# Kernel tuning notes

Hardware: AMD Instinct MI355X
Metric: run time of the kernel (lower is better)

The kernel has to match this reference:

```python
import jax, jax.numpy as jnp
import numpy as np

N, K, M, C, OUT, S = 80000, 8, 1000, 128, 64, 2
EPS = 1e-5


def _bn(x, g, b, m, v):
    # eval-mode BatchNorm1d applied over the last (channel) axis
    return (x - m) * (g / jnp.sqrt(v + EPS)) + b


def setup_inputs() -> dict:
    key = jax.random.key(0)
    ks = jax.random.split(key, 40)
    it = iter(range(40))
    rn = lambda sh, s=1.0: jax.random.normal(ks[next(it)], sh, dtype=jnp.float32) * s
    ru = lambda sh: jax.random.uniform(ks[next(it)], sh, dtype=jnp.float32, minval=0.5, maxval=1.5)
    w = 0.05
    inp = {}
    inp["sp_fea"] = rn((M, C))
    inp["sp_xyz"] = rn((M, 3))
    inp["o_p_fea"] = rn((N, C))
    inp["p_xyz"] = rn((N, 3))
    # linear_q / linear_k / linear_v  (in_planes -> mid_planes)
    inp["Wq"] = rn((C, C), w); inp["bq"] = jnp.zeros((C,), jnp.float32)
    inp["Wk"] = rn((C, C), w); inp["bk"] = jnp.zeros((C,), jnp.float32)
    inp["Wv"] = rn((C, C), w); inp["bv"] = jnp.zeros((C,), jnp.float32)
    # linear_p: Linear(3,3) -> BN(3) -> ReLU -> Linear(3, mid)
    inp["Wp1"] = rn((3, 3), 0.5); inp["bp1"] = jnp.zeros((3,), jnp.float32)
    inp["gp"] = 1.0 + rn((3,), 0.1); inp["betap"] = rn((3,), 0.1)
    inp["mp"] = rn((3,), 0.1); inp["vp"] = ru((3,))
    inp["Wp2"] = rn((3, C), 0.3); inp["bp2"] = jnp.zeros((C,), jnp.float32)
    # linear_w: BN(mid) -> ReLU -> Linear(mid,out) -> BN(out) -> ReLU -> Linear(out,out)
    inp["g1"] = 1.0 + rn((C,), 0.1); inp["beta1"] = rn((C,), 0.1)
    inp["m1"] = rn((C,), 0.1); inp["v1"] = ru((C,))
    inp["W1"] = rn((C, OUT), w); inp["b1"] = jnp.zeros((OUT,), jnp.float32)
    inp["g2"] = 1.0 + rn((OUT,), 0.1); inp["beta2"] = rn((OUT,), 0.1)
    inp["m2"] = rn((OUT,), 0.1); inp["v2"] = ru((OUT,))
    inp["W2"] = rn((OUT, OUT), w); inp["b2"] = jnp.zeros((OUT,), jnp.float32)
    # index / offset inputs (ints)
    inp["c2p_idx_abs"] = jax.random.randint(ks[next(it)], (N, K), 0, M)
    inp["c2p_idx"] = jax.random.randint(ks[next(it)], (N, K), 0, M)
    inp["cluster_idx"] = jax.random.randint(ks[next(it)], (N,), 0, M)
    inp["offset"] = jnp.array([N], dtype=jnp.int32)
    inp["sp_offset"] = jnp.array([M], dtype=jnp.int32)
    return inp


def reference(sp_fea, sp_xyz, o_p_fea, p_xyz,
              Wq, bq, Wk, bk, Wv, bv,
              Wp1, bp1, gp, betap, mp, vp, Wp2, bp2,
              g1, beta1, m1, v1, W1, b1,
              g2, beta2, m2, v2, W2, b2,
              c2p_idx_abs, c2p_idx, cluster_idx, offset, sp_offset):
    q = o_p_fea @ Wq + bq                               # [N, C]
    k_sp = (sp_fea @ Wk + bk)[c2p_idx_abs]              # gather -> [N, K, C]
    v_sp = (sp_fea @ Wv + bv)[c2p_idx_abs]              # [N, K, C]
    p_e = sp_xyz[c2p_idx_abs]                           # [N, K, 3]
    # positional encoding MLP
    p_e = jax.nn.relu(_bn(p_e @ Wp1 + bp1, gp, betap, mp, vp)) @ Wp2 + bp2  # [N, K, C]
    # vector attention scores
    w = k_sp - q[:, None, :] + p_e                      # [N, K, C]
    w = jax.nn.relu(_bn(w, g1, beta1, m1, v1)) @ W1 + b1
    w = jax.nn.relu(_bn(w, g2, beta2, m2, v2)) @ W2 + b2  # [N, K, OUT]
    w = jax.nn.softmax(w, axis=1)                        # softmax over the K neighbors
    # shared-plane weighted sum
    bi = ((v_sp + p_e).reshape(N, K, S, C // S) * w[:, :, None, :]).reshape(N, K, C)
    bi = bi.sum(axis=2)                                  # [N, K]
    return jax.nn.softmax(bi, axis=1)                    # association matrix [N, K]
```

## Files before the change

### kernel.cpp

```cpp
#include <hip/hip_runtime.h>
#include <stdint.h>

#define EPS 1e-5f

#define NPTS 80000
#define CDIM 128
#define ODIM 64
#define KNBR 8
#define MSUP 1000

#define KP2_OFF  0
#define UT_OFF   (512*1024)
#define WQF_OFF  (768*1024)
#define W1F_OFF  (800*1024)
#define W2F_OFF  (816*1024)
#define C1_OFF   (824*1024)

typedef float f32x4 __attribute__((ext_vector_type(4)));
typedef short bf16x8 __attribute__((ext_vector_type(8)));

union FragU { bf16x8 v; unsigned u[4]; };

__device__ inline unsigned pack_rne(float lo, float hi) {
  unsigned a = __builtin_bit_cast(unsigned, lo);
  unsigned b = __builtin_bit_cast(unsigned, hi);
  a += 0x7FFFu + ((a >> 16) & 1u);
  b += 0x7FFFu + ((b >> 16) & 1u);
  return (a >> 16) | (b & 0xFFFF0000u);
}

__global__ __launch_bounds__(256)
void k_tables(const float* __restrict__ sp_fea, const float* __restrict__ sp_xyz,
              const float* __restrict__ Wk, const float* __restrict__ bk,
              const float* __restrict__ Wv, const float* __restrict__ bv,
              const float* __restrict__ Wp1, const float* __restrict__ bp1,
              const float* __restrict__ gp, const float* __restrict__ betap,
              const float* __restrict__ mp, const float* __restrict__ vp,
              const float* __restrict__ Wp2, const float* __restrict__ bp2,
              const float* __restrict__ g1, const float* __restrict__ beta1,
              const float* __restrict__ m1, const float* __restrict__ v1,
              const float* __restrict__ bq, char* __restrict__ ws)
{
  float* kp2 = (float*)(ws + KP2_OFF);
  float* uT  = (float*)(ws + UT_OFF);
  const int t = threadIdx.x;
  const int c = t & 127;
  const int half = t >> 7;
  __shared__ float fea[2][128];
  __shared__ float vpsh[2][128];
  for (int i = 0; i < 2; ++i) {
    const int m = blockIdx.x * 4 + half * 2 + i;
    fea[half][c] = sp_fea[m * 128 + c];
    const float x0 = sp_xyz[m*3+0], x1 = sp_xyz[m*3+1], x2 = sp_xyz[m*3+2];
    float pe = bp2[c];
    #pragma unroll
    for (int ii = 0; ii < 3; ++ii) {
      float s = bp1[ii] + x0*Wp1[0*3+ii] + x1*Wp1[1*3+ii] + x2*Wp1[2*3+ii];
      s = (s - mp[ii]) * (gp[ii] * rsqrtf(vp[ii] + EPS)) + betap[ii];
      s = fmaxf(s, 0.0f);
      pe += s * Wp2[ii*128 + c];
    }
    __syncthreads();
    float kv = bk[c], vv = bv[c];
    #pragma unroll 4
    for (int d = 0; d < 128; ++d) {
      const float f = fea[half][d];
      kv = fmaf(f, Wk[d*128 + c], kv);
      vv = fmaf(f, Wv[d*128 + c], vv);
    }
    const float s1c = g1[c] * rsqrtf(v1[c] + EPS);
    kp2[m*128 + c] = (kv + pe - m1[c] - bq[c]) * s1c + beta1[c];
    vpsh[half][c] = vv + pe;
    __syncthreads();
    if (c < 64) uT[m*64 + c] = vpsh[half][c] + vpsh[half][c + 64];
    __syncthreads();
  }
}

__global__ __launch_bounds__(256)
void k_swz(const float* __restrict__ Wq, const float* __restrict__ W1, const float* __restrict__ W2,
           const float* __restrict__ g1, const float* __restrict__ v1,
           const float* __restrict__ g2, const float* __restrict__ v2,
           const float* __restrict__ b1, const float* __restrict__ m2,
           const float* __restrict__ beta2, char* __restrict__ ws)
{
  const int tid = blockIdx.x * 256 + threadIdx.x;
  if (tid < 2048) {
    const int e = tid, f = e >> 6, l = e & 63;
    const int kt = f >> 3, mt = f & 7;
    const int c = mt*16 + (l & 15);
    const int d0 = kt*32 + (l >> 4)*8;
    const float sc = g1[c] * rsqrtf(v1[c] + EPS);
    uint4 u;
    u.x = pack_rne(Wq[(d0+0)*128 + c]*sc, Wq[(d0+1)*128 + c]*sc);
    u.y = pack_rne(Wq[(d0+2)*128 + c]*sc, Wq[(d0+3)*128 + c]*sc);
    u.z = pack_rne(Wq[(d0+4)*128 + c]*sc, Wq[(d0+5)*128 + c]*sc);
    u.w = pack_rne(Wq[(d0+6)*128 + c]*sc, Wq[(d0+7)*128 + c]*sc);
    *(uint4*)(ws + WQF_OFF + e*16) = u;
  } else if (tid < 3072) {
    const int e = tid - 2048, f = e >> 6, l = e & 63;
    const int kt = f >> 2, jt = f & 3;
    const int j = jt*16 + (l & 15);
    const int c0 = kt*32 + (l >> 4)*8;
    const float sc = g2[j] * rsqrtf(v2[j] + EPS);
    uint4 u;
    u.x = pack_rne(W1[(c0+0)*64 + j]*sc, W1[(c0+1)*64 + j]*sc);
    u.y = pack_rne(W1[(c0+2)*64 + j]*sc, W1[(c0+3)*64 + j]*sc);
    u.z = pack_rne(W1[(c0+4)*64 + j]*sc, W1[(c0+5)*64 + j]*sc);
    u.w = pack_rne(W1[(c0+6)*64 + j]*sc, W1[(c0+7)*64 + j]*sc);
    *(uint4*)(ws + W1F_OFF + e*16) = u;
  } else if (tid < 3584) {
    const int e = tid - 3072, f = e >> 6, l = e & 63;
    const int kt2 = f >> 2, nt = f & 3;
    const int jp = nt*16 + (l & 15);
    const int j0 = kt2*32 + (l >> 4)*8;
    uint4 u;
    u.x = pack_rne(W2[(j0+0)*64 + jp], W2[(j0+1)*64 + jp]);
    u.y = pack_rne(W2[(j0+2)*64 + jp], W2[(j0+3)*64 + jp]);
    u.z = pack_rne(W2[(j0+4)*64 + jp], W2[(j0+5)*64 + jp]);
    u.w = pack_rne(W2[(j0+6)*64 + jp], W2[(j0+7)*64 + jp]);
    *(uint4*)(ws + W2F_OFF + e*16) = u;
  } else if (tid < 3648) {
    const int j = tid - 3584;
    const float sc = g2[j] * rsqrtf(v2[j] + EPS);
    ((float*)(ws + C1_OFF))[j] = (b1[j] - m2[j]) * sc + beta2[j];
  }
}

#define LDS_QS_PITCH 528
#define LDS_QS_SIZE  (16*528)
#define LDS_H2_PITCH 144
#define LDS_H2_SIZE  (16*144)

__global__ __launch_bounds__(256, 2)
void k_main(const float* __restrict__ o_p_fea, const int* __restrict__ idx,
            const float* __restrict__ b2, const char* __restrict__ ws,
            float* __restrict__ out)
{
  const float*  kp2 = (const float*)(ws + KP2_OFF);
  const float*  uT  = (const float*)(ws + UT_OFF);
  const bf16x8* wqf = (const bf16x8*)(ws + WQF_OFF);
  const bf16x8* w1f = (const bf16x8*)(ws + W1F_OFF);
  const bf16x8* w2f = (const bf16x8*)(ws + W2F_OFF);
  const float*  c1  = (const float*)(ws + C1_OFF);

  __shared__ __align__(16) char lds[4*LDS_QS_SIZE + 4*LDS_H2_SIZE];
  const int wave = threadIdx.x >> 6;
  const int l = threadIdx.x & 63;
  const int quad = l >> 4, row = l & 15;
  char* qs_w = lds + wave * LDS_QS_SIZE;
  char* h2_w = lds + 4*LDS_QS_SIZE + wave * LDS_H2_SIZE;

  const int sg = blockIdx.x * 4 + wave;
  const int n0 = sg * 16;

  bf16x8 w1r[16];
  #pragma unroll
  for (int f = 0; f < 16; ++f) w1r[f] = w1f[f*64 + l];
  bf16x8 w2r[8];
  #pragma unroll
  for (int f = 0; f < 8; ++f) w2r[f] = w2f[f*64 + l];
  f32x4 c1r[4];
  #pragma unroll
  for (int jt = 0; jt < 4; ++jt) c1r[jt] = *(const f32x4*)(c1 + jt*16 + quad*4);
  float b2r[4];
  #pragma unroll
  for (int nt = 0; nt < 4; ++nt) b2r[nt] = b2[row + nt*16];

  f32x4 qa[8];
  #pragma unroll
  for (int mt = 0; mt < 8; ++mt) qa[mt] = (f32x4){0.f, 0.f, 0.f, 0.f};
  const float* feab = o_p_fea + (size_t)(n0 + row) * 128;
  #pragma unroll
  for (int kt = 0; kt < 4; ++kt) {
    f32x4 fa = *(const f32x4*)(feab + kt*32 + quad*8);
    f32x4 fb = *(const f32x4*)(feab + kt*32 + quad*8 + 4);
    FragU bu;
    bu.u[0] = pack_rne(fa[0], fa[1]);
    bu.u[1] = pack_rne(fa[2], fa[3]);
    bu.u[2] = pack_rne(fb[0], fb[1]);
    bu.u[3] = pack_rne(fb[2], fb[3]);
    #pragma unroll
    for (int mt = 0; mt < 8; ++mt)
      qa[mt] = __builtin_amdgcn_mfma_f32_16x16x32_bf16(wqf[(kt*8+mt)*64 + l], bu.v, qa[mt], 0, 0, 0);
  }
  #pragma unroll
  for (int mt = 0; mt < 8; ++mt)
    *(f32x4*)(qs_w + row*LDS_QS_PITCH + (mt*16 + quad*4)*4) = qa[mt];

  const int idx_base = n0 * 8;
  #pragma unroll 1
  for (int g = 0; g < 8; ++g) {
    const int m_r = idx[idx_base + g*16 + row];
    const int nloc = row >> 3;
    const float* qrow = (const float*)(qs_w + (g*2 + nloc) * LDS_QS_PITCH);

    f32x4 a1[4];
    #pragma unroll
    for (int jt = 0; jt < 4; ++jt) a1[jt] = (f32x4){0.f, 0.f, 0.f, 0.f};
    #pragma unroll
    for (int kt = 0; kt < 4; ++kt) {
      const int c8 = kt*32 + quad*8;
      const float* kr = kp2 + (size_t)m_r * 128 + c8;
      f32x4 ka = *(const f32x4*)kr;
      f32x4 kb = *(const f32x4*)(kr + 4);
      f32x4 q0 = *(const f32x4*)(qrow + c8);
      f32x4 q1 = *(const f32x4*)(qrow + c8 + 4);
      const float x0 = fmaxf(ka[0]-q0[0], 0.f), x1 = fmaxf(ka[1]-q0[1], 0.f);
      const float x2 = fmaxf(ka[2]-q0[2], 0.f), x3 = fmaxf(ka[3]-q0[3], 0.f);
      const float x4 = fmaxf(kb[0]-q1[0], 0.f), x5 = fmaxf(kb[1]-q1[1], 0.f);
      const float x6 = fmaxf(kb[2]-q1[2], 0.f), x7 = fmaxf(kb[3]-q1[3], 0.f);
      FragU xf;
      xf.u[0] = pack_rne(x0, x1); xf.u[1] = pack_rne(x2, x3);
      xf.u[2] = pack_rne(x4, x5); xf.u[3] = pack_rne(x6, x7);
      #pragma unroll
      for (int jt = 0; jt < 4; ++jt)
        a1[jt] = __builtin_amdgcn_mfma_f32_16x16x32_bf16(w1r[kt*4+jt], xf.v, a1[jt], 0, 0, 0);
    }
    #pragma unroll
    for (int jt = 0; jt < 4; ++jt) {
      f32x4 v = a1[jt] + c1r[jt];
      uint2 pp;
      pp.x = pack_rne(fmaxf(v[0], 0.f), fmaxf(v[1], 0.f));
      pp.y = pack_rne(fmaxf(v[2], 0.f), fmaxf(v[3], 0.f));
      *(uint2*)(h2_w + row*LDS_H2_PITCH + (jt*16 + quad*4)*2) = pp;
    }

    f32x4 a2[4];
    #pragma unroll
    for (int nt = 0; nt < 4; ++nt) a2[nt] = (f32x4){0.f, 0.f, 0.f, 0.f};
    #pragma unroll
    for (int kt2 = 0; kt2 < 2; ++kt2) {
      bf16x8 af = *(const bf16x8*)(h2_w + row*LDS_H2_PITCH + (kt2*32 + quad*8)*2);
      #pragma unroll
      for (int nt = 0; nt < 4; ++nt)
        a2[nt] = __builtin_amdgcn_mfma_f32_16x16x32_bf16(af, w2r[kt2*4+nt], a2[nt], 0, 0, 0);
    }
    float e[4][4], rs[4];
    #pragma unroll
    for (int nt = 0; nt < 4; ++nt) {
      #pragma unroll
      for (int rg = 0; rg < 4; ++rg) e[nt][rg] = __expf(a2[nt][rg] + b2r[nt]);
      float s = e[nt][0] + e[nt][1] + e[nt][2] + e[nt][3];
      s += __shfl_xor(s, 16);
      rs[nt] = __builtin_amdgcn_rcpf(s);
    }
    int msrc[4];
    #pragma unroll
    for (int rg = 0; rg < 4; ++rg) msrc[rg] = __shfl(m_r, quad*4 + rg);
    float bi[4] = {0.f, 0.f, 0.f, 0.f};
    #pragma unroll
    for (int rg = 0; rg < 4; ++rg) {
      const float* urow = uT + (size_t)msrc[rg] * 64 + row;
      #pragma unroll
      for (int nt = 0; nt < 4; ++nt)
        bi[rg] = fmaf(e[nt][rg] * rs[nt], urow[nt*16], bi[rg]);
    }
    #pragma unroll
    for (int rg = 0; rg < 4; ++rg) {
      float b = bi[rg];
      b += __shfl_xor(b, 1);
      b += __shfl_xor(b, 2);
      b += __shfl_xor(b, 4);
      b += __shfl_xor(b, 8);
      bi[rg] = b;
    }
    const float eb0 = __expf(bi[0]), eb1 = __expf(bi[1]);
    const float eb2 = __expf(bi[2]), eb3 = __expf(bi[3]);
    float sb = eb0 + eb1 + eb2 + eb3;
    sb += __shfl_xor(sb, 16);
    const float rsb = __builtin_amdgcn_rcpf(sb);
    if (row < 4) {
      const float vsel = row == 0 ? eb0 : row == 1 ? eb1 : row == 2 ? eb2 : eb3;
      out[n0*8 + g*16 + quad*4 + row] = vsel * rsb;
    }
  }
}

extern "C" void kernel_launch(void* const* d_in, const int* in_sizes, int n_in,
                              void* d_out, int out_size, void* d_ws, size_t ws_size,
                              hipStream_t stream)
{
  const float* sp_fea  = (const float*)d_in[0];
  const float* sp_xyz  = (const float*)d_in[1];
  const float* o_p_fea = (const float*)d_in[2];
  const float* Wq    = (const float*)d_in[4];
  const float* bq    = (const float*)d_in[5];
  const float* Wk    = (const float*)d_in[6];
  const float* bk    = (const float*)d_in[7];
  const float* Wv    = (const float*)d_in[8];
  const float* bv    = (const float*)d_in[9];
  const float* Wp1   = (const float*)d_in[10];
  const float* bp1   = (const float*)d_in[11];
  const float* gp    = (const float*)d_in[12];
  const float* betap = (const float*)d_in[13];
  const float* mp    = (const float*)d_in[14];
  const float* vp    = (const float*)d_in[15];
  const float* Wp2   = (const float*)d_in[16];
  const float* bp2   = (const float*)d_in[17];
  const float* g1    = (const float*)d_in[18];
  const float* beta1 = (const float*)d_in[19];
  const float* m1    = (const float*)d_in[20];
  const float* v1    = (const float*)d_in[21];
  const float* W1    = (const float*)d_in[22];
  const float* b1    = (const float*)d_in[23];
  const float* g2    = (const float*)d_in[24];
  const float* beta2 = (const float*)d_in[25];
  const float* m2    = (const float*)d_in[26];
  const float* v2    = (const float*)d_in[27];
  const float* W2    = (const float*)d_in[28];
  const float* b2    = (const float*)d_in[29];
  const int* c2p_idx_abs = (const int*)d_in[30];

  char* ws = (char*)d_ws;
  float* out = (float*)d_out;

  hipLaunchKernelGGL(k_tables, dim3(250), dim3(256), 0, stream,
                     sp_fea, sp_xyz, Wk, bk, Wv, bv, Wp1, bp1, gp, betap, mp, vp,
                     Wp2, bp2, g1, beta1, m1, v1, bq, ws);
  hipLaunchKernelGGL(k_swz, dim3(15), dim3(256), 0, stream,
                     Wq, W1, W2, g1, v1, g2, v2, b1, m2, beta2, ws);
  hipLaunchKernelGGL(k_main, dim3(1250), dim3(256), 0, stream,
                     o_p_fea, c2p_idx_abs, b2, ws, out);
}
```

Measured before the change: 228.5 us.

## Merge prep kernels, use one-wave main blocks, prefetch indices, use hardware bf16 convert

The two preprocessing kernels become one launch. The table part now uses one block per supernode and splits the 128-deep K/V reduction across two half-blocks. The main kernel moves from 256-thread blocks of four waves to 64-thread single-wave blocks with a larger grid. It prefetches all eight neighbor index rows up front and loads the W1/W2 fragments after the q GEMM, which may shorten register live ranges. Float-to-bf16 packing uses the hardware cvt_pk_bf16 builtin when the compiler offers it, falling back to manual round-to-nearest-even.

```diff
diff --git a/kernel.cpp b/kernel.cpp
--- a/kernel.cpp
+++ b/kernel.cpp
@@ -21,109 +21,122 @@
 
 union FragU { bf16x8 v; unsigned u[4]; };
 
-__device__ inline unsigned pack_rne(float lo, float hi) {
+#if __has_builtin(__builtin_amdgcn_cvt_pk_bf16_f32)
+typedef __bf16 bf16x2_t __attribute__((ext_vector_type(2)));
+#define HAVE_PK_BF16 1
+#endif
+
+__device__ inline unsigned pk_bf16(float lo, float hi) {
+#ifdef HAVE_PK_BF16
+  return __builtin_bit_cast(unsigned, __builtin_amdgcn_cvt_pk_bf16_f32(lo, hi));
+#else
   unsigned a = __builtin_bit_cast(unsigned, lo);
   unsigned b = __builtin_bit_cast(unsigned, hi);
   a += 0x7FFFu + ((a >> 16) & 1u);
   b += 0x7FFFu + ((b >> 16) & 1u);
   return (a >> 16) | (b & 0xFFFF0000u);
+#endif
 }
 
 __global__ __launch_bounds__(256)
-void k_tables(const float* __restrict__ sp_fea, const float* __restrict__ sp_xyz,
-              const float* __restrict__ Wk, const float* __restrict__ bk,
-              const float* __restrict__ Wv, const float* __restrict__ bv,
-              const float* __restrict__ Wp1, const float* __restrict__ bp1,
-              const float* __restrict__ gp, const float* __restrict__ betap,
-              const float* __restrict__ mp, const float* __restrict__ vp,
-              const float* __restrict__ Wp2, const float* __restrict__ bp2,
-              const float* __restrict__ g1, const float* __restrict__ beta1,
-              const float* __restrict__ m1, const float* __restrict__ v1,
-              const float* __restrict__ bq, char* __restrict__ ws)
+void k_prep(const float* __restrict__ sp_fea, const float* __restrict__ sp_xyz,
+            const float* __restrict__ Wk, const float* __restrict__ bk,
+            const float* __restrict__ Wv, const float* __restrict__ bv,
+            const float* __restrict__ Wp1, const float* __restrict__ bp1,
+            const float* __restrict__ gp, const float* __restrict__ betap,
+            const float* __restrict__ mp, const float* __restrict__ vp,
+            const float* __restrict__ Wp2, const float* __restrict__ bp2,
+            const float* __restrict__ g1, const float* __restrict__ beta1,
+            const float* __restrict__ m1, const float* __restrict__ v1,
+            const float* __restrict__ bq,
+            const float* __restrict__ Wq, const float* __restrict__ W1,
+            const float* __restrict__ W2,
+            const float* __restrict__ g2, const float* __restrict__ v2,
+            const float* __restrict__ b1, const float* __restrict__ m2,
+            const float* __restrict__ beta2, char* __restrict__ ws)
 {
-  float* kp2 = (float*)(ws + KP2_OFF);
-  float* uT  = (float*)(ws + UT_OFF);
-  const int t = threadIdx.x;
-  const int c = t & 127;
-  const int half = t >> 7;
-  __shared__ float fea[2][128];
-  __shared__ float vpsh[2][128];
-  for (int i = 0; i < 2; ++i) {
-    const int m = blockIdx.x * 4 + half * 2 + i;
-    fea[half][c] = sp_fea[m * 128 + c];
-    const float x0 = sp_xyz[m*3+0], x1 = sp_xyz[m*3+1], x2 = sp_xyz[m*3+2];
-    float pe = bp2[c];
-    #pragma unroll
-    for (int ii = 0; ii < 3; ++ii) {
-      float s = bp1[ii] + x0*Wp1[0*3+ii] + x1*Wp1[1*3+ii] + x2*Wp1[2*3+ii];
-      s = (s - mp[ii]) * (gp[ii] * rsqrtf(vp[ii] + EPS)) + betap[ii];
-      s = fmaxf(s, 0.0f);
-      pe += s * Wp2[ii*128 + c];
-    }
+  if (blockIdx.x < 1000) {
+    float* kp2 = (float*)(ws + KP2_OFF);
+    float* uT  = (float*)(ws + UT_OFF);
+    const int m = blockIdx.x;
+    const int t = threadIdx.x;
+    const int c = t & 127, half = t >> 7;
+    __shared__ float fea[128];
+    __shared__ float pk[128], pv[128];
+    if (t < 128) fea[t] = sp_fea[m * 128 + t];
     __syncthreads();
-    float kv = bk[c], vv = bv[c];
-    #pragma unroll 4
-    for (int d = 0; d < 128; ++d) {
-      const float f = fea[half][d];
-      kv = fmaf(f, Wk[d*128 + c], kv);
-      vv = fmaf(f, Wv[d*128 + c], vv);
-    }
-    const float s1c = g1[c] * rsqrtf(v1[c] + EPS);
-    kp2[m*128 + c] = (kv + pe - m1[c] - bq[c]) * s1c + beta1[c];
-    vpsh[half][c] = vv + pe;
+    float kv = 0.f, vv = 0.f;
+    const float* wkc = Wk + half * 64 * 128 + c;
+    const float* wvc = Wv + half * 64 * 128 + c;
+    const float* feah = fea + half * 64;
+    #pragma unroll 8
+    for (int d = 0; d < 64; ++d) {
+      const float f = feah[d];
+      kv = fmaf(f, wkc[d * 128], kv);
+      vv = fmaf(f, wvc[d * 128], vv);
+    }
+    if (half) { pk[c] = kv; pv[c] = vv; }
     __syncthreads();
-    if (c < 64) uT[m*64 + c] = vpsh[half][c] + vpsh[half][c + 64];
+    if (!half) {
+      kv += pk[c] + bk[c];
+      vv += pv[c] + bv[c];
+      const float x0 = sp_xyz[m*3+0], x1 = sp_xyz[m*3+1], x2 = sp_xyz[m*3+2];
+      float pe = bp2[c];
+      #pragma unroll
+      for (int ii = 0; ii < 3; ++ii) {
+        float s = bp1[ii] + x0*Wp1[0*3+ii] + x1*Wp1[1*3+ii] + x2*Wp1[2*3+ii];
+        s = (s - mp[ii]) * (gp[ii] * rsqrtf(vp[ii] + EPS)) + betap[ii];
+        s = fmaxf(s, 0.0f);
+        pe += s * Wp2[ii*128 + c];
+      }
+      const float s1c = g1[c] * rsqrtf(v1[c] + EPS);
+      kp2[m*128 + c] = (kv + pe - m1[c] - bq[c]) * s1c + beta1[c];
+      pv[c] = vv + pe;
+    }
     __syncthreads();
-  }
-}
-
-__global__ __launch_bounds__(256)
-void k_swz(const float* __restrict__ Wq, const float* __restrict__ W1, const float* __restrict__ W2,
-           const float* __restrict__ g1, const float* __restrict__ v1,
-           const float* __restrict__ g2, const float* __restrict__ v2,
-           const float* __restrict__ b1, const float* __restrict__ m2,
-           const float* __restrict__ beta2, char* __restrict__ ws)
-{
-  const int tid = blockIdx.x * 256 + threadIdx.x;
-  if (tid < 2048) {
-    const int e = tid, f = e >> 6, l = e & 63;
-    const int kt = f >> 3, mt = f & 7;
-    const int c = mt*16 + (l & 15);
-    const int d0 = kt*32 + (l >> 4)*8;
-    const float sc = g1[c] * rsqrtf(v1[c] + EPS);
-    uint4 u;
-    u.x = pack_rne(Wq[(d0+0)*128 + c]*sc, Wq[(d0+1)*128 + c]*sc);
-    u.y = pack_rne(Wq[(d0+2)*128 + c]*sc, Wq[(d0+3)*128 + c]*sc);
-    u.z = pack_rne(Wq[(d0+4)*128 + c]*sc, Wq[(d0+5)*128 + c]*sc);
-    u.w = pack_rne(Wq[(d0+6)*128 + c]*sc, Wq[(d0+7)*128 + c]*sc);
-    *(uint4*)(ws + WQF_OFF + e*16) = u;
-  } else if (tid < 3072) {
-    const int e = tid - 2048, f = e >> 6, l = e & 63;
-    const int kt = f >> 2, jt = f & 3;
-    const int j = jt*16 + (l & 15);
-    const int c0 = kt*32 + (l >> 4)*8;
-    const float sc = g2[j] * rsqrtf(v2[j] + EPS);
-    uint4 u;
-    u.x = pack_rne(W1[(c0+0)*64 + j]*sc, W1[(c0+1)*64 + j]*sc);
-    u.y = pack_rne(W1[(c0+2)*64 + j]*sc, W1[(c0+3)*64 + j]*sc);
-    u.z = pack_rne(W1[(c0+4)*64 + j]*sc, W1[(c0+5)*64 + j]*sc);
-    u.w = pack_rne(W1[(c0+6)*64 + j]*sc, W1[(c0+7)*64 + j]*sc);
-    *(uint4*)(ws + W1F_OFF + e*16) = u;
-  } else if (tid < 3584) {
-    const int e = tid - 3072, f = e >> 6, l = e & 63;
-    const int kt2 = f >> 2, nt = f & 3;
-    const int jp = nt*16 + (l & 15);
-    const int j0 = kt2*32 + (l >> 4)*8;
-    uint4 u;
-    u.x = pack_rne(W2[(j0+0)*64 + jp], W2[(j0+1)*64 + jp]);
-    u.y = pack_rne(W2[(j0+2)*64 + jp], W2[(j0+3)*64 + jp]);
-    u.z = pack_rne(W2[(j0+4)*64 + jp], W2[(j0+5)*64 + jp]);
-    u.w = pack_rne(W2[(j0+6)*64 + jp], W2[(j0+7)*64 + jp]);
-    *(uint4*)(ws + W2F_OFF + e*16) = u;
-  } else if (tid < 3648) {
-    const int j = tid - 3584;
-    const float sc = g2[j] * rsqrtf(v2[j] + EPS);
-    ((float*)(ws + C1_OFF))[j] = (b1[j] - m2[j]) * sc + beta2[j];
+    if (t < 64) uT[m*64 + t] = pv[t] + pv[t + 64];
+  } else {
+    const int tid = (blockIdx.x - 1000) * 256 + threadIdx.x;
+    if (tid < 2048) {
+      const int e = tid, f = e >> 6, l = e & 63;
+      const int kt = f >> 3, mt = f & 7;
+      const int c = mt*16 + (l & 15);
+      const int d0 = kt*32 + (l >> 4)*8;
+      const float sc = g1[c] * rsqrtf(v1[c] + EPS);
+      uint4 u;
+      u.x = pk_bf16(Wq[(d0+0)*128 + c]*sc, Wq[(d0+1)*128 + c]*sc);
+      u.y = pk_bf16(Wq[(d0+2)*128 + c]*sc, Wq[(d0+3)*128 + c]*sc);
+      u.z = pk_bf16(Wq[(d0+4)*128 + c]*sc, Wq[(d0+5)*128 + c]*sc);
+      u.w = pk_bf16(Wq[(d0+6)*128 + c]*sc, Wq[(d0+7)*128 + c]*sc);
+      *(uint4*)(ws + WQF_OFF + e*16) = u;
+    } else if (tid < 3072) {
+      const int e = tid - 2048, f = e >> 6, l = e & 63;
+      const int kt = f >> 2, jt = f & 3;
+      const int j = jt*16 + (l & 15);
+      const int c0 = kt*32 + (l >> 4)*8;
+      const float sc = g2[j] * rsqrtf(v2[j] + EPS);
+      uint4 u;
+      u.x = pk_bf16(W1[(c0+0)*64 + j]*sc, W1[(c0+1)*64 + j]*sc);
+      u.y = pk_bf16(W1[(c0+2)*64 + j]*sc, W1[(c0+3)*64 + j]*sc);
+      u.z = pk_bf16(W1[(c0+4)*64 + j]*sc, W1[(c0+5)*64 + j]*sc);
+      u.w = pk_bf16(W1[(c0+6)*64 + j]*sc, W1[(c0+7)*64 + j]*sc);
+      *(uint4*)(ws + W1F_OFF + e*16) = u;
+    } else if (tid < 3584) {
+      const int e = tid - 3072, f = e >> 6, l = e & 63;
+      const int kt2 = f >> 2, nt = f & 3;
+      const int jp = nt*16 + (l & 15);
+      const int j0 = kt2*32 + (l >> 4)*8;
+      uint4 u;
+      u.x = pk_bf16(W2[(j0+0)*64 + jp], W2[(j0+1)*64 + jp]);
+      u.y = pk_bf16(W2[(j0+2)*64 + jp], W2[(j0+3)*64 + jp]);
+      u.z = pk_bf16(W2[(j0+4)*64 + jp], W2[(j0+5)*64 + jp]);
+      u.w = pk_bf16(W2[(j0+6)*64 + jp], W2[(j0+7)*64 + jp]);
+      *(uint4*)(ws + W2F_OFF + e*16) = u;
+    } else if (tid < 3648) {
+      const int j = tid - 3584;
+      const float sc = g2[j] * rsqrtf(v2[j] + EPS);
+      ((float*)(ws + C1_OFF))[j] = (b1[j] - m2[j]) * sc + beta2[j];
+    }
   }
 }
 
@@ -132,7 +145,7 @@
 #define LDS_H2_PITCH 144
 #define LDS_H2_SIZE  (16*144)
 
-__global__ __launch_bounds__(256, 2)
+__global__ __launch_bounds__(64, 3)
 void k_main(const float* __restrict__ o_p_fea, const int* __restrict__ idx,
             const float* __restrict__ b2, const char* __restrict__ ws,
             float* __restrict__ out)
@@ -144,28 +157,18 @@
   const bf16x8* w2f = (const bf16x8*)(ws + W2F_OFF);
   const float*  c1  = (const float*)(ws + C1_OFF);
 
-  __shared__ __align__(16) char lds[4*LDS_QS_SIZE + 4*LDS_H2_SIZE];
-  const int wave = threadIdx.x >> 6;
-  const int l = threadIdx.x & 63;
+  __shared__ __align__(16) char lds[LDS_QS_SIZE + LDS_H2_SIZE];
+  char* qs_w = lds;
+  char* h2_w = lds + LDS_QS_SIZE;
+
+  const int l = threadIdx.x;
   const int quad = l >> 4, row = l & 15;
-  char* qs_w = lds + wave * LDS_QS_SIZE;
-  char* h2_w = lds + 4*LDS_QS_SIZE + wave * LDS_H2_SIZE;
-
-  const int sg = blockIdx.x * 4 + wave;
-  const int n0 = sg * 16;
-
-  bf16x8 w1r[16];
-  #pragma unroll
-  for (int f = 0; f < 16; ++f) w1r[f] = w1f[f*64 + l];
-  bf16x8 w2r[8];
-  #pragma unroll
-  for (int f = 0; f < 8; ++f) w2r[f] = w2f[f*64 + l];
-  f32x4 c1r[4];
-  #pragma unroll
-  for (int jt = 0; jt < 4; ++jt) c1r[jt] = *(const f32x4*)(c1 + jt*16 + quad*4);
-  float b2r[4];
-  #pragma unroll
-  for (int nt = 0; nt < 4; ++nt) b2r[nt] = b2[row + nt*16];
+  const int n0 = blockIdx.x * 16;
+  const int idx_base = n0 * 8;
+
+  int mr8[8];
+  #pragma unroll
+  for (int g = 0; g < 8; ++g) mr8[g] = idx[idx_base + g*16 + row];
 
   f32x4 qa[8];
   #pragma unroll
@@ -176,10 +179,10 @@
     f32x4 fa = *(const f32x4*)(feab + kt*32 + quad*8);
     f32x4 fb = *(const f32x4*)(feab + kt*32 + quad*8 + 4);
     FragU bu;
-    bu.u[0] = pack_rne(fa[0], fa[1]);
-    bu.u[1] = pack_rne(fa[2], fa[3]);
-    bu.u[2] = pack_rne(fb[0], fb[1]);
-    bu.u[3] = pack_rne(fb[2], fb[3]);
+    bu.u[0] = pk_bf16(fa[0], fa[1]);
+    bu.u[1] = pk_bf16(fa[2], fa[3]);
+    bu.u[2] = pk_bf16(fb[0], fb[1]);
+    bu.u[3] = pk_bf16(fb[2], fb[3]);
     #pragma unroll
     for (int mt = 0; mt < 8; ++mt)
       qa[mt] = __builtin_amdgcn_mfma_f32_16x16x32_bf16(wqf[(kt*8+mt)*64 + l], bu.v, qa[mt], 0, 0, 0);
@@ -188,10 +191,22 @@
   for (int mt = 0; mt < 8; ++mt)
     *(f32x4*)(qs_w + row*LDS_QS_PITCH + (mt*16 + quad*4)*4) = qa[mt];
 
-  const int idx_base = n0 * 8;
+  bf16x8 w1r[16];
+  #pragma unroll
+  for (int f = 0; f < 16; ++f) w1r[f] = w1f[f*64 + l];
+  bf16x8 w2r[8];
+  #pragma unroll
+  for (int f = 0; f < 8; ++f) w2r[f] = w2f[f*64 + l];
+  f32x4 c1r[4];
+  #pragma unroll
+  for (int jt = 0; jt < 4; ++jt) c1r[jt] = *(const f32x4*)(c1 + jt*16 + quad*4);
+  float b2r[4];
+  #pragma unroll
+  for (int nt = 0; nt < 4; ++nt) b2r[nt] = b2[row + nt*16];
+
   #pragma unroll 1
   for (int g = 0; g < 8; ++g) {
-    const int m_r = idx[idx_base + g*16 + row];
+    const int m_r = mr8[g];
     const int nloc = row >> 3;
     const float* qrow = (const float*)(qs_w + (g*2 + nloc) * LDS_QS_PITCH);
 
@@ -211,8 +226,8 @@
       const float x4 = fmaxf(kb[0]-q1[0], 0.f), x5 = fmaxf(kb[1]-q1[1], 0.f);
       const float x6 = fmaxf(kb[2]-q1[2], 0.f), x7 = fmaxf(kb[3]-q1[3], 0.f);
       FragU xf;
-      xf.u[0] = pack_rne(x0, x1); xf.u[1] = pack_rne(x2, x3);
-      xf.u[2] = pack_rne(x4, x5); xf.u[3] = pack_rne(x6, x7);
+      xf.u[0] = pk_bf16(x0, x1); xf.u[1] = pk_bf16(x2, x3);
+      xf.u[2] = pk_bf16(x4, x5); xf.u[3] = pk_bf16(x6, x7);
       #pragma unroll
       for (int jt = 0; jt < 4; ++jt)
         a1[jt] = __builtin_amdgcn_mfma_f32_16x16x32_bf16(w1r[kt*4+jt], xf.v, a1[jt], 0, 0, 0);
@@ -221,8 +236,8 @@
     for (int jt = 0; jt < 4; ++jt) {
       f32x4 v = a1[jt] + c1r[jt];
       uint2 pp;
-      pp.x = pack_rne(fmaxf(v[0], 0.f), fmaxf(v[1], 0.f));
-      pp.y = pack_rne(fmaxf(v[2], 0.f), fmaxf(v[3], 0.f));
+      pp.x = pk_bf16(fmaxf(v[0], 0.f), fmaxf(v[1], 0.f));
+      pp.y = pk_bf16(fmaxf(v[2], 0.f), fmaxf(v[3], 0.f));
       *(uint2*)(h2_w + row*LDS_H2_PITCH + (jt*16 + quad*4)*2) = pp;
     }
 
@@ -315,11 +330,10 @@
   char* ws = (char*)d_ws;
   float* out = (float*)d_out;
 
-  hipLaunchKernelGGL(k_tables, dim3(250), dim3(256), 0, stream,
+  hipLaunchKernelGGL(k_prep, dim3(1015), dim3(256), 0, stream,
                      sp_fea, sp_xyz, Wk, bk, Wv, bv, Wp1, bp1, gp, betap, mp, vp,
-                     Wp2, bp2, g1, beta1, m1, v1, bq, ws);
-  hipLaunchKernelGGL(k_swz, dim3(15), dim3(256), 0, stream,
-                     Wq, W1, W2, g1, v1, g2, v2, b1, m2, beta2, ws);
-  hipLaunchKernelGGL(k_main, dim3(1250), dim3(256), 0, stream,
+                     Wp2, bp2, g1, beta1, m1, v1, bq,
+                     Wq, W1, W2, g2, v2, b1, m2, beta2, ws);
+  hipLaunchKernelGGL(k_main, dim3(5000), dim3(64), 0, stream,
                      o_p_fea, c2p_idx_abs, b2, ws, out);
 }
```

After: 245.4 us. +7.4%, slower.
